# Performance work log

Hardware: AMD Instinct MI355X
Metric: run time of the kernel (lower is better)

## Reference

```python
import jax, jax.numpy as jnp
import numpy as np

N = 100000
E = 3200000
IN_F = 256
OUT_F = 256
CLAMP = 10.0


def setup_inputs() -> dict:
    key = jax.random.key(0)
    k1, k2, k3, k4, k5 = jax.random.split(key, 5)
    x = jax.random.normal(k1, (N, IN_F), dtype=jnp.float32)
    adj_rows = jnp.sort(jax.random.randint(k2, (E,), 0, N, dtype=jnp.int32))
    adj_cols = jax.random.randint(k3, (E,), 0, N, dtype=jnp.int32)
    adj_vals = jax.random.uniform(k4, (E,), dtype=jnp.float32)
    # glorot-ish init (scaled by 0.1 as in the module)
    stdv = 0.1 * np.sqrt(6.0 / (IN_F + OUT_F))
    weight = jax.random.uniform(k5, (IN_F, OUT_F), dtype=jnp.float32,
                                minval=-stdv, maxval=stdv)
    bias = jnp.zeros((OUT_F,), dtype=jnp.float32)
    return {"x": x, "adj_rows": adj_rows, "adj_cols": adj_cols,
            "adj_vals": adj_vals, "weight": weight, "bias": bias}


def reference(x, adj_rows, adj_cols, adj_vals, weight, bias):
    # clamp input
    x = jnp.clip(x, -CLAMP, CLAMP)
    # dense projection: [N, in] @ [in, out]
    support = jnp.clip(x @ weight, -CLAMP, CLAMP)
    # sparse adjacency SpMM: out[r] += val * support[c] for each edge (r, c)
    msgs = adj_vals[:, None] * support[adj_cols]          # [E, out]
    output = jax.ops.segment_sum(msgs, adj_rows, num_segments=N)
    output = jnp.clip(output, -CLAMP, CLAMP)
    output = output + bias
    output = jax.nn.relu(output)
    return jnp.clip(output, -CLAMP, CLAMP)
```

## Files before the change

kernel.cpp:

```cpp
#include <hip/hip_runtime.h>

#define N_NODES 100000
#define N_EDGES 3200000
#define IN_F    256
#define OUT_F   256
#define CLAMP_V 10.0f

typedef __attribute__((ext_vector_type(8))) short bf16x8;
typedef __attribute__((ext_vector_type(4))) float f32x4;

__device__ __forceinline__ float clampf(float v) {
    return fminf(fmaxf(v, -CLAMP_V), CLAMP_V);
}
__device__ __forceinline__ unsigned f2bf(float f) {
    unsigned u = __float_as_uint(f);
    u += 0x7fffu + ((u >> 16) & 1u);
    return u >> 16;
}
__device__ __forceinline__ unsigned cvt_pk_bf16(float lo, float hi) {
    unsigned r;
    asm("v_cvt_pk_bf16_f32 %0, %1, %2" : "=v"(r) : "v"(lo), "v"(hi));
    return r;
}
__device__ __forceinline__ float bflo(unsigned w) { return __uint_as_float(w << 16); }
__device__ __forceinline__ float bfhi(unsigned w) { return __uint_as_float(w & 0xffff0000u); }

__global__ __launch_bounds__(256) void prep(
    const float* __restrict__ w, unsigned short* __restrict__ wt,
    const int* __restrict__ rows, int* __restrict__ row_ptr) {
    const int bid = blockIdx.x;
    if (bid < 256) {
        int i = bid * 256 + threadIdx.x;
        int k = i & 255, n = i >> 8;
        float v = w[(size_t)k * OUT_F + n];
        int dst = ((k >> 3) << 11) + (n << 3) + (k & 7);
        wt[dst] = (unsigned short)f2bf(v);
    } else {
        int r = (bid - 256) * 256 + threadIdx.x;
        if (r > N_NODES) return;
        int lo = 0, hi = N_EDGES;
        while (lo < hi) {
            int mid = (lo + hi) >> 1;
            if (rows[mid] < r) lo = mid + 1; else hi = mid;
        }
        row_ptr[r] = lo;
    }
}

__global__ __launch_bounds__(256) void gemm_mfma(
    const float* __restrict__ x, const unsigned short* __restrict__ wt,
    unsigned* __restrict__ sup8, float* __restrict__ scales) {
    __shared__ char lds[32768];

    const int t    = threadIdx.x;
    const int lane = t & 63;
    const int wc   = t >> 6;
    const int l15  = lane & 15;
    const int l4   = lane >> 4;
    const int blockRow = blockIdx.x * 64;

    const int srow = t >> 2;
    const int sqt  = t & 3;
    int sgrow = blockRow + srow; if (sgrow >= N_NODES) sgrow = N_NODES - 1;
    const float* sbase = x + (size_t)sgrow * IN_F + sqt * 16;
    int woff[4];
    #pragma unroll
    for (int j = 0; j < 4; ++j) {
        int chunk = sqt * 4 + j;
        woff[j] = srow * 256 + ((chunk ^ (srow & 15)) << 4);
    }

    f32x4 st[4];
    #pragma unroll
    for (int j = 0; j < 4; ++j)
        st[j] = *(const f32x4*)(sbase + j * 4);

    f32x4 acc[4][4];
    #pragma unroll
    for (int m = 0; m < 4; ++m)
        #pragma unroll
        for (int n = 0; n < 4; ++n)
            acc[m][n] = (f32x4)0.f;

    #pragma unroll
    for (int s = 0; s < 4; ++s) {
        char* buf = lds + (s & 1) * 16384;
        #pragma unroll
        for (int j = 0; j < 4; ++j)
            *(f32x4*)(buf + woff[j]) = st[j];
        if (s < 3) {
            const float* nb = sbase + (s + 1) * 64;
            #pragma unroll
            for (int j = 0; j < 4; ++j)
                st[j] = *(const f32x4*)(nb + j * 4);
        }
        __syncthreads();

        #pragma unroll
        for (int kk = 0; kk < 2; ++kk) {
            bf16x8 a[4], b[4];
            #pragma unroll
            for (int m = 0; m < 4; ++m) {
                const int row = m * 16 + l15;
                const int c0 = (kk * 8 + l4 * 2 + 0) ^ l15;
                const int c1 = (kk * 8 + l4 * 2 + 1) ^ l15;
                f32x4 u0 = *(const f32x4*)(buf + row * 256 + (c0 << 4));
                f32x4 u1 = *(const f32x4*)(buf + row * 256 + (c1 << 4));
                union { unsigned u[4]; bf16x8 v; } pk;
                pk.u[0] = cvt_pk_bf16(clampf(u0[0]), clampf(u0[1]));
                pk.u[1] = cvt_pk_bf16(clampf(u0[2]), clampf(u0[3]));
                pk.u[2] = cvt_pk_bf16(clampf(u1[0]), clampf(u1[1]));
                pk.u[3] = cvt_pk_bf16(clampf(u1[2]), clampf(u1[3]));
                a[m] = pk.v;
            }
            const int kg = s * 8 + kk * 4 + l4;
            #pragma unroll
            for (int n = 0; n < 4; ++n)
                b[n] = *(const bf16x8*)(wt + (kg << 11) + ((wc * 64 + n * 16 + l15) << 3));
            #pragma unroll
            for (int m = 0; m < 4; ++m)
                #pragma unroll
                for (int n = 0; n < 4; ++n)
                    acc[m][n] = __builtin_amdgcn_mfma_f32_16x16x32_bf16(
                        a[m], b[n], acc[m][n], 0, 0, 0);
        }
    }
    __syncthreads();

    {
        char* sl = lds;
        #pragma unroll
        for (int m = 0; m < 4; ++m) {
            #pragma unroll
            for (int n = 0; n < 4; ++n) {
                int col2 = (wc * 64 + n * 16 + l15) * 2;
                #pragma unroll
                for (int r = 0; r < 4; ++r) {
                    int row = m * 16 + l4 * 4 + r;
                    int off = row * 512 + (col2 ^ (((row >> 2) & 3) << 4));
                    *(unsigned short*)(sl + off) = (unsigned short)f2bf(clampf(acc[m][n][r]));
                }
            }
        }
    }
    __syncthreads();

    {
        const uint4* sl4 = (const uint4*)lds;
        const int row = t >> 2;
        const int qt  = t & 3;
        const int swz = (row >> 2) & 3;

        uint4 c[8];
        float mx = 0.f;
        #pragma unroll
        for (int j = 0; j < 8; ++j) {
            c[j] = sl4[row * 32 + ((qt * 8 + j) ^ swz)];
            const unsigned* cu = (const unsigned*)&c[j];
            #pragma unroll
            for (int q = 0; q < 4; ++q)
                mx = fmaxf(mx, fmaxf(fabsf(bflo(cu[q])), fabsf(bfhi(cu[q]))));
        }
        mx = fmaxf(mx, __shfl_xor(mx, 1));
        mx = fmaxf(mx, __shfl_xor(mx, 2));

        const float inv = 127.f / fmaxf(mx, 1e-30f);
        const int grow = blockRow + row;
        if (grow < N_NODES) {
            unsigned p[16];
            #pragma unroll
            for (int j = 0; j < 8; ++j) {
                const unsigned* cu = (const unsigned*)&c[j];
                #pragma unroll
                for (int q = 0; q < 2; ++q) {
                    unsigned b0 = (unsigned)(int)rintf(bflo(cu[q*2+0]) * inv) + 128u;
                    unsigned b1 = (unsigned)(int)rintf(bfhi(cu[q*2+0]) * inv) + 128u;
                    unsigned b2 = (unsigned)(int)rintf(bflo(cu[q*2+1]) * inv) + 128u;
                    unsigned b3 = (unsigned)(int)rintf(bfhi(cu[q*2+1]) * inv) + 128u;
                    p[j*2+q] = b0 | (b1 << 8) | (b2 << 16) | (b3 << 24);
                }
            }
            uint4* dst = (uint4*)(sup8 + (size_t)grow * 64 + qt * 16);
            #pragma unroll
            for (int j = 0; j < 4; ++j)
                dst[j] = *(const uint4*)&p[j * 4];
            if (qt == 0) scales[grow] = mx * (1.f / 127.f);
        }
    }
}

#define FMAQ(g, vs)                                                       \
    S += (vs);                                                            \
    acc[0] += (vs) * (float)((g).x & 0xffu);                              \
    acc[1] += (vs) * (float)(((g).x >> 8) & 0xffu);                       \
    acc[2] += (vs) * (float)(((g).x >> 16) & 0xffu);                      \
    acc[3] += (vs) * (float)((g).x >> 24);                                \
    acc[4] += (vs) * (float)((g).y & 0xffu);                              \
    acc[5] += (vs) * (float)(((g).y >> 8) & 0xffu);                       \
    acc[6] += (vs) * (float)(((g).y >> 16) & 0xffu);                      \
    acc[7] += (vs) * (float)((g).y >> 24);

__global__ __launch_bounds__(256) void spmm_out(
    const unsigned* __restrict__ sup8, const float* __restrict__ scales,
    const int* __restrict__ row_ptr, const int* __restrict__ cols,
    const float* __restrict__ vals, const float* __restrict__ bias,
    float* __restrict__ out) {
    const int wid  = threadIdx.x >> 6;
    const int lane = threadIdx.x & 63;
    const int row  = blockIdx.x * 4 + wid;
    if (row >= N_NODES) return;

    const int e0   = row_ptr[row];
    const int e1   = row_ptr[row + 1];
    const int half = lane >> 5;
    const int c32  = lane & 31;

    const uint2* sup2 = (const uint2*)sup8;
    float acc[8] = {0.f,0.f,0.f,0.f,0.f,0.f,0.f,0.f};
    float S = 0.f;

    int e = e0;
    for (; e + 8 <= e1; e += 8) {
        int   ea = e + half, eb = ea + 2, ec = ea + 4, ed = ea + 6;
        int   ca = cols[ea], cb = cols[eb], cc = cols[ec], cd = cols[ed];
        float va = vals[ea], vb = vals[eb], vc = vals[ec], vd = vals[ed];
        float vsa = va * scales[ca], vsb = vb * scales[cb];
        float vsc = vc * scales[cc], vsd = vd * scales[cd];
        uint2 ga = sup2[(size_t)ca * 32 + c32];
        uint2 gb = sup2[(size_t)cb * 32 + c32];
        uint2 gc = sup2[(size_t)cc * 32 + c32];
        uint2 gd = sup2[(size_t)cd * 32 + c32];
        FMAQ(ga, vsa); FMAQ(gb, vsb); FMAQ(gc, vsc); FMAQ(gd, vsd);
    }
    for (; e + 4 <= e1; e += 4) {
        int   ea = e + half, eb = ea + 2;
        int   ca = cols[ea], cb = cols[eb];
        float va = vals[ea], vb = vals[eb];
        float vsa = va * scales[ca], vsb = vb * scales[cb];
        uint2 ga = sup2[(size_t)ca * 32 + c32];
        uint2 gb = sup2[(size_t)cb * 32 + c32];
        FMAQ(ga, vsa); FMAQ(gb, vsb);
    }
    for (; e < e1; e += 2) {
        int   ea = e + half;
        bool  ok = ea < e1;
        int   ca = cols[ok ? ea : e];
        float va = ok ? vals[ea] : 0.f;
        float vsa = va * scales[ca];
        uint2 ga = sup2[(size_t)ca * 32 + c32];
        FMAQ(ga, vsa);
    }

    S *= 128.f;
    #pragma unroll
    for (int j = 0; j < 8; ++j)
        acc[j] -= S;

    #pragma unroll
    for (int j = 0; j < 8; ++j)
        acc[j] += __shfl_xor(acc[j], 32);

    const float4 b4 = ((const float4*)bias)[c32 * 2 + half];
    f32x4 o;
    o.x = fminf(fmaxf(clampf(acc[half * 4 + 0]) + b4.x, 0.f), CLAMP_V);
    o.y = fminf(fmaxf(clampf(acc[half * 4 + 1]) + b4.y, 0.f), CLAMP_V);
    o.z = fminf(fmaxf(clampf(acc[half * 4 + 2]) + b4.z, 0.f), CLAMP_V);
    o.w = fminf(fmaxf(clampf(acc[half * 4 + 3]) + b4.w, 0.f), CLAMP_V);
    __builtin_nontemporal_store(o, (f32x4*)(out + (size_t)row * OUT_F + c32 * 8 + half * 4));
}

extern "C" void kernel_launch(void* const* d_in, const int* in_sizes, int n_in,
                              void* d_out, int out_size, void* d_ws, size_t ws_size,
                              hipStream_t stream) {
    const float* x        = (const float*)d_in[0];
    const int*   adj_rows = (const int*)d_in[1];
    const int*   adj_cols = (const int*)d_in[2];
    const float* adj_vals = (const float*)d_in[3];
    const float* weight   = (const float*)d_in[4];
    const float* bias     = (const float*)d_in[5];
    float*       out      = (float*)d_out;

    char* ws = (char*)d_ws;
    unsigned*       sup8    = (unsigned*)ws;
    float*          scales  = (float*)(ws + 25600000);
    int*            row_ptr = (int*)(ws + 26000000);
    unsigned short* wt      = (unsigned short*)(ws + 26400064);

    const int rp_blocks = (N_NODES + 1 + 255) / 256;
    prep<<<256 + rp_blocks, 256, 0, stream>>>(weight, wt, adj_rows, row_ptr);
    gemm_mfma<<<(N_NODES + 63) / 64, 256, 0, stream>>>(x, wt, sup8, scales);
    spmm_out<<<(N_NODES + 3) / 4, 256, 0, stream>>>(sup8, scales, row_ptr,
                                                    adj_cols, adj_vals, bias, out);
}
```

Before: 174.3 us.

## Gather 16-byte int8 feature chunks per lane with four edges per wavefront step

The SpMM kernel now has each lane load a uint4 (16 int8 features) instead of a uint2. The wavefront splits into four quarter-groups that each handle a different edge, so four edges are processed in parallel per step and 16 per unrolled iteration. The partial sums are reduced across quarters with two xor shuffles, and the scale correction is applied afterwards. The aim is wider gather loads and fewer loop iterations, in exchange for 16 accumulators per lane, more shuffles and a less efficient tail on rows with few edges.

```diff
diff --git a/kernel.cpp b/kernel.cpp
--- a/kernel.cpp
+++ b/kernel.cpp
@@ -189,16 +189,24 @@
     }
 }
 
-#define FMAQ(g, vs)                                                       \
+#define FMAQ16(g, vs)                                                     \
     S += (vs);                                                            \
-    acc[0] += (vs) * (float)((g).x & 0xffu);                              \
-    acc[1] += (vs) * (float)(((g).x >> 8) & 0xffu);                       \
-    acc[2] += (vs) * (float)(((g).x >> 16) & 0xffu);                      \
-    acc[3] += (vs) * (float)((g).x >> 24);                                \
-    acc[4] += (vs) * (float)((g).y & 0xffu);                              \
-    acc[5] += (vs) * (float)(((g).y >> 8) & 0xffu);                       \
-    acc[6] += (vs) * (float)(((g).y >> 16) & 0xffu);                      \
-    acc[7] += (vs) * (float)((g).y >> 24);
+    acc[ 0] += (vs) * (float)((g).x & 0xffu);                             \
+    acc[ 1] += (vs) * (float)(((g).x >> 8) & 0xffu);                      \
+    acc[ 2] += (vs) * (float)(((g).x >> 16) & 0xffu);                     \
+    acc[ 3] += (vs) * (float)((g).x >> 24);                               \
+    acc[ 4] += (vs) * (float)((g).y & 0xffu);                             \
+    acc[ 5] += (vs) * (float)(((g).y >> 8) & 0xffu);                      \
+    acc[ 6] += (vs) * (float)(((g).y >> 16) & 0xffu);                     \
+    acc[ 7] += (vs) * (float)((g).y >> 24);                               \
+    acc[ 8] += (vs) * (float)((g).z & 0xffu);                             \
+    acc[ 9] += (vs) * (float)(((g).z >> 8) & 0xffu);                      \
+    acc[10] += (vs) * (float)(((g).z >> 16) & 0xffu);                     \
+    acc[11] += (vs) * (float)((g).z >> 24);                               \
+    acc[12] += (vs) * (float)((g).w & 0xffu);                             \
+    acc[13] += (vs) * (float)(((g).w >> 8) & 0xffu);                      \
+    acc[14] += (vs) * (float)(((g).w >> 16) & 0xffu);                     \
+    acc[15] += (vs) * (float)((g).w >> 24);
 
 __global__ __launch_bounds__(256) void spmm_out(
     const unsigned* __restrict__ sup8, const float* __restrict__ scales,
@@ -210,63 +218,65 @@
     const int row  = blockIdx.x * 4 + wid;
     if (row >= N_NODES) return;
 
-    const int e0   = row_ptr[row];
-    const int e1   = row_ptr[row + 1];
-    const int half = lane >> 5;
-    const int c32  = lane & 31;
-
-    const uint2* sup2 = (const uint2*)sup8;
-    float acc[8] = {0.f,0.f,0.f,0.f,0.f,0.f,0.f,0.f};
+    const int e0 = row_ptr[row];
+    const int e1 = row_ptr[row + 1];
+    const int q  = lane >> 4;
+    const int fl = lane & 15;
+
+    const uint4* sup16 = (const uint4*)sup8;
+    float acc[16];
+    #pragma unroll
+    for (int j = 0; j < 16; ++j) acc[j] = 0.f;
     float S = 0.f;
 
     int e = e0;
-    for (; e + 8 <= e1; e += 8) {
-        int   ea = e + half, eb = ea + 2, ec = ea + 4, ed = ea + 6;
-        int   ca = cols[ea], cb = cols[eb], cc = cols[ec], cd = cols[ed];
-        float va = vals[ea], vb = vals[eb], vc = vals[ec], vd = vals[ed];
-        float vsa = va * scales[ca], vsb = vb * scales[cb];
-        float vsc = vc * scales[cc], vsd = vd * scales[cd];
-        uint2 ga = sup2[(size_t)ca * 32 + c32];
-        uint2 gb = sup2[(size_t)cb * 32 + c32];
-        uint2 gc = sup2[(size_t)cc * 32 + c32];
-        uint2 gd = sup2[(size_t)cd * 32 + c32];
-        FMAQ(ga, vsa); FMAQ(gb, vsb); FMAQ(gc, vsc); FMAQ(gd, vsd);
+    for (; e + 16 <= e1; e += 16) {
+        int   i0 = e + q, i1 = i0 + 4, i2 = i0 + 8, i3 = i0 + 12;
+        int   c0 = cols[i0], c1 = cols[i1], c2 = cols[i2], c3 = cols[i3];
+        float v0 = vals[i0], v1 = vals[i1], v2 = vals[i2], v3 = vals[i3];
+        float s0 = v0 * scales[c0], s1 = v1 * scales[c1];
+        float s2 = v2 * scales[c2], s3 = v3 * scales[c3];
+        uint4 g0 = sup16[(size_t)c0 * 16 + fl];
+        uint4 g1 = sup16[(size_t)c1 * 16 + fl];
+        uint4 g2 = sup16[(size_t)c2 * 16 + fl];
+        uint4 g3 = sup16[(size_t)c3 * 16 + fl];
+        FMAQ16(g0, s0); FMAQ16(g1, s1); FMAQ16(g2, s2); FMAQ16(g3, s3);
     }
     for (; e + 4 <= e1; e += 4) {
-        int   ea = e + half, eb = ea + 2;
-        int   ca = cols[ea], cb = cols[eb];
-        float va = vals[ea], vb = vals[eb];
-        float vsa = va * scales[ca], vsb = vb * scales[cb];
-        uint2 ga = sup2[(size_t)ca * 32 + c32];
-        uint2 gb = sup2[(size_t)cb * 32 + c32];
-        FMAQ(ga, vsa); FMAQ(gb, vsb);
-    }
-    for (; e < e1; e += 2) {
-        int   ea = e + half;
-        bool  ok = ea < e1;
-        int   ca = cols[ok ? ea : e];
-        float va = ok ? vals[ea] : 0.f;
-        float vsa = va * scales[ca];
-        uint2 ga = sup2[(size_t)ca * 32 + c32];
-        FMAQ(ga, vsa);
-    }
+        int   i0 = e + q;
+        int   c0 = cols[i0];
+        float v0 = vals[i0];
+        float s0 = v0 * scales[c0];
+        uint4 g0 = sup16[(size_t)c0 * 16 + fl];
+        FMAQ16(g0, s0);
+    }
+    if (e < e1) {
+        int   i0 = e + q;
+        bool  ok = i0 < e1;
+        int   c0 = cols[ok ? i0 : e];
+        float v0 = ok ? vals[i0] : 0.f;
+        float s0 = v0 * scales[c0];
+        uint4 g0 = sup16[(size_t)c0 * 16 + fl];
+        FMAQ16(g0, s0);
+    }
+
+    #pragma unroll
+    for (int j = 0; j < 16; ++j) {
+        acc[j] += __shfl_xor(acc[j], 16);
+        acc[j] += __shfl_xor(acc[j], 32);
+    }
+    S += __shfl_xor(S, 16);
+    S += __shfl_xor(S, 32);
 
     S *= 128.f;
-    #pragma unroll
-    for (int j = 0; j < 8; ++j)
-        acc[j] -= S;
-
-    #pragma unroll
-    for (int j = 0; j < 8; ++j)
-        acc[j] += __shfl_xor(acc[j], 32);
-
-    const float4 b4 = ((const float4*)bias)[c32 * 2 + half];
+
+    const float4 b4 = ((const float4*)bias)[fl * 4 + q];
     f32x4 o;
-    o.x = fminf(fmaxf(clampf(acc[half * 4 + 0]) + b4.x, 0.f), CLAMP_V);
-    o.y = fminf(fmaxf(clampf(acc[half * 4 + 1]) + b4.y, 0.f), CLAMP_V);
-    o.z = fminf(fmaxf(clampf(acc[half * 4 + 2]) + b4.z, 0.f), CLAMP_V);
-    o.w = fminf(fmaxf(clampf(acc[half * 4 + 3]) + b4.w, 0.f), CLAMP_V);
-    __builtin_nontemporal_store(o, (f32x4*)(out + (size_t)row * OUT_F + c32 * 8 + half * 4));
+    o.x = fminf(fmaxf(clampf(acc[q * 4 + 0] - S) + b4.x, 0.f), CLAMP_V);
+    o.y = fminf(fmaxf(clampf(acc[q * 4 + 1] - S) + b4.y, 0.f), CLAMP_V);
+    o.z = fminf(fmaxf(clampf(acc[q * 4 + 2] - S) + b4.z, 0.f), CLAMP_V);
+    o.w = fminf(fmaxf(clampf(acc[q * 4 + 3] - S) + b4.w, 0.f), CLAMP_V);
+    __builtin_nontemporal_store(o, (f32x4*)(out + (size_t)row * OUT_F + fl * 16 + q * 4));
 }
 
 extern "C" void kernel_launch(void* const* d_in, const int* in_sizes, int n_in,
```

Measured after the change: 193.5 us. 11.0% more time.
